# Optimization experiments

Measured on AMD Instinct MI355X. Metric: run time of the kernel, lower is better.

## Reference

```python
import jax, jax.numpy as jnp
import numpy as np

K = 1024      # num_embeddings
D = 256       # embedding_dim
BETA = 0.25
DECAY = 0.99
EPS = 1e-05


def setup_inputs() -> dict:
    key = jax.random.key(0)
    k1, k2 = jax.random.split(key)
    z_e = jax.random.normal(k1, (32, D, 32, 32), dtype=jnp.float32)
    embedding = jax.random.normal(k2, (K, D), dtype=jnp.float32)
    ema_cluster_size = jnp.zeros((K,), dtype=jnp.float32)
    ema_w = embedding  # buffer initialized as a clone of the codebook
    return {"z_e": z_e, "embedding": embedding,
            "ema_cluster_size": ema_cluster_size, "ema_w": ema_w}


def reference(z_e, embedding, ema_cluster_size, ema_w):
    B, Dd, H, W = z_e.shape
    # (B, D, H, W) -> (N, D)
    flat_z = jnp.transpose(z_e, (0, 2, 3, 1)).reshape(-1, Dd)

    # L2 distance argmin (||z||^2 + ||e||^2 - 2 z.e)
    dist = (jnp.sum(flat_z * flat_z, axis=1, keepdims=True)
            + jnp.sum(embedding * embedding, axis=1)
            - 2.0 * flat_z @ embedding.T)
    indices = jnp.argmin(dist, axis=1)  # (N,)

    # EMA update (operates on detached values; buffers updated in-place in torch)
    flat_z_sg = jax.lax.stop_gradient(flat_z)
    cluster_size = jax.ops.segment_sum(
        jnp.ones_like(indices, dtype=z_e.dtype), indices, num_segments=K)
    new_ema_cluster_size = DECAY * ema_cluster_size + (1.0 - DECAY) * cluster_size
    dw = jax.ops.segment_sum(flat_z_sg, indices, num_segments=K)  # one_hot.T @ flat_z
    new_ema_w = DECAY * ema_w + (1.0 - DECAY) * dw
    new_embedding = new_ema_w / (new_ema_cluster_size + EPS)[:, None]

    # Gather uses the *updated* codebook (torch copies into the buffer first)
    z_q_flat = new_embedding[indices]                      # (N, D)
    z_q = jnp.transpose(z_q_flat.reshape(B, H, W, Dd), (0, 3, 1, 2))

    # Straight-through estimator + commitment loss
    z_q_st = z_e + jax.lax.stop_gradient(z_q - z_e)
    vq_loss = BETA * jnp.mean((z_e - jax.lax.stop_gradient(z_q)) ** 2)

    return (z_q_st, vq_loss, indices.reshape(B, H, W),
            new_embedding, new_ema_cluster_size, new_ema_w)
```

## Files before the change

kernel.cpp:

```cpp
#include <hip/hip_runtime.h>
#include <stdint.h>

#define N_ROWS 32768
#define K_CODES 1024
#define D_DIM 256
#define NELEM 8388608

#define WS_COUNTS 0
#define WS_LOSS 1030
#define WS_ENORM 263168
#define WS_ROWBEST_BYTES 1056768
#define WS_IDX_BYTES 1318912

#define O_ZQ 0
#define O_LOSS 8388608
#define O_IDX 8388609
#define O_EMB 8421377
#define O_CS 8683521
#define O_EMAW 8684545

#define EP_BYTE_OFF 33685520

typedef _Float16 half8 __attribute__((ext_vector_type(8)));
typedef float f32x16 __attribute__((ext_vector_type(16)));

__device__ __forceinline__ unsigned int fenc(float f) {
    unsigned int u = __float_as_uint(f);
    return (u & 0x80000000u) ? ~u : (u | 0x80000000u);
}
__device__ __forceinline__ unsigned long long umin64(unsigned long long a, unsigned long long b) {
    return a < b ? a : b;
}
__device__ __forceinline__ void gll16(const void* g, void* l) {
    __builtin_amdgcn_global_load_lds((const __attribute__((address_space(1))) void*)g,
                                     (__attribute__((address_space(3))) void*)l, 16, 0, 0);
}

__global__ __launch_bounds__(256) void k_init(float* ws) {
    int i = blockIdx.x * 256 + threadIdx.x;
    if (i < 2048) ws[i] = 0.0f;
    unsigned long long* rb = (unsigned long long*)((char*)ws + WS_ROWBEST_BYTES);
    if (i < N_ROWS) rb[i] = 0xFFFFFFFFFFFFFFFFull;
}

__global__ __launch_bounds__(256) void k_conv_e(const float* __restrict__ emb,
                                                _Float16* __restrict__ Ep,
                                                float* __restrict__ enorm) {
    int k = blockIdx.x, d = threadIdx.x;
    float v = emb[k * 256 + d];
    _Float16 h = (_Float16)v;
    _Float16 l = (_Float16)(v - (float)h);
    int s = d >> 3, sub = d & 7;
    Ep[((size_t)s * 1024 + k) * 8 + sub] = h;
    Ep[((size_t)(32 + s) * 1024 + k) * 8 + sub] = l;
    float sq = v * v;
    #pragma unroll
    for (int off = 32; off >= 1; off >>= 1) sq += __shfl_down(sq, off, 64);
    __shared__ float red[4];
    if ((d & 63) == 0) red[d >> 6] = sq;
    __syncthreads();
    if (d == 0) enorm[k] = (red[0] + red[1]) + (red[2] + red[3]);
}

__global__ __launch_bounds__(256) void k_conv_z(const float* __restrict__ z_e,
                                                _Float16* __restrict__ Zp,
                                                float* __restrict__ lossacc) {
    __shared__ float lt[64 * 68];
    __shared__ float red[4];
    int t = threadIdx.x;
    int hw0 = blockIdx.x * 64, d0 = blockIdx.y * 64, b = blockIdx.z;
    const float* src = z_e + (size_t)b * 262144 + (size_t)d0 * 1024 + hw0;
    int dl = t >> 4, hl = (t & 15) * 4;
    float sq = 0.0f;
    #pragma unroll
    for (int i = 0; i < 4; i++) {
        int d = dl + i * 16;
        float4 v = *(const float4*)(src + (size_t)d * 1024 + hl);
        sq += v.x * v.x + v.y * v.y + v.z * v.z + v.w * v.w;
        lt[(hl + 0) * 68 + d] = v.x;
        lt[(hl + 1) * 68 + d] = v.y;
        lt[(hl + 2) * 68 + d] = v.z;
        lt[(hl + 3) * 68 + d] = v.w;
    }
    __syncthreads();
    int hr = t >> 2, seg = t & 3;
    int n = b * 1024 + hw0 + hr;
    int sg0 = (d0 >> 3) + seg * 2;
    half8 hi[2], lo[2];
    #pragma unroll
    for (int p = 0; p < 2; p++) {
        #pragma unroll
        for (int j = 0; j < 8; j++) {
            float v = lt[hr * 68 + seg * 16 + p * 8 + j];
            _Float16 h = (_Float16)v;
            hi[p][j] = h;
            lo[p][j] = (_Float16)(v - (float)h);
        }
    }
    *(half8*)(Zp + ((size_t)(sg0 + 0) * 32768 + n) * 8) = hi[0];
    *(half8*)(Zp + ((size_t)(sg0 + 1) * 32768 + n) * 8) = hi[1];
    *(half8*)(Zp + ((size_t)(32 + sg0) * 32768 + n) * 8) = lo[0];
    *(half8*)(Zp + ((size_t)(33 + sg0) * 32768 + n) * 8) = lo[1];
    #pragma unroll
    for (int off = 32; off >= 1; off >>= 1) sq += __shfl_down(sq, off, 64);
    if ((t & 63) == 0) red[t >> 6] = sq;
    __syncthreads();
    if (t == 0) atomicAdd(lossacc, (red[0] + red[1]) + (red[2] + red[3]));
}

__global__ __launch_bounds__(256) void k_mm(const _Float16* __restrict__ Zp,
                                            const _Float16* __restrict__ Ep,
                                            const float* __restrict__ enorm,
                                            unsigned long long* __restrict__ row_best) {
    __shared__ __align__(16) char smem[32768];
    _Float16* Za = (_Float16*)smem;
    _Float16* Ea = (_Float16*)(smem + 16384);
    unsigned long long* slot = (unsigned long long*)smem;

    int t = threadIdx.x;
    int lane = t & 63, wv = t >> 6;
    int b = blockIdx.x;
    int rt = (b & 7) + ((b >> 6) << 3);
    int ct = (b >> 3) & 7;
    int row0 = rt * 128, code0 = ct * 128;

    int wr = wv >> 1, wc = wv & 1;
    int m31 = lane & 31, ko = lane >> 5;

    f32x16 acc[2][2];
    #pragma unroll
    for (int i = 0; i < 2; i++)
        #pragma unroll
        for (int j = 0; j < 2; j++)
            #pragma unroll
            for (int r = 0; r < 16; r++) acc[i][j][r] = 0.0f;

    const char* zgl = (const char*)Zp + ((size_t)(2 * wv) * 32768 + row0 + lane) * 16;
    const char* egl = (const char*)Ep + ((size_t)(2 * wv) * 1024 + code0 + lane) * 16;
    _Float16* zld = Za + 2 * wv * 1024;
    _Float16* eld = Ea + 2 * wv * 1024;

    for (int c = 0; c < 12; c++) {
        int kz = (c < 8) ? c : (c - 8);
        int ge = (c < 4) ? c * 8 : (c < 8) ? (c - 4) * 8 : 32 + (c - 8) * 8;
        const char* zg = zgl + (size_t)kz * 8 * 32768 * 16;
        const char* eg = egl + (size_t)ge * 1024 * 16;
        gll16(zg, zld);
        gll16(zg + 64 * 16, zld + 512);
        gll16(zg + 32768 * 16, zld + 1024);
        gll16(zg + 32768 * 16 + 64 * 16, zld + 1536);
        gll16(eg, eld);
        gll16(eg + 64 * 16, eld + 512);
        gll16(eg + 1024 * 16, eld + 1024);
        gll16(eg + 1024 * 16 + 64 * 16, eld + 1536);
        __syncthreads();
        #pragma unroll
        for (int ks = 0; ks < 4; ks++) {
            int sseg = 2 * ks + ko;
            half8 a0 = *(const half8*)(Za + sseg * 1024 + (wr * 64 + m31) * 8);
            half8 a1 = *(const half8*)(Za + sseg * 1024 + (wr * 64 + 32 + m31) * 8);
            half8 b0 = *(const half8*)(Ea + sseg * 1024 + (wc * 64 + m31) * 8);
            half8 b1 = *(const half8*)(Ea + sseg * 1024 + (wc * 64 + 32 + m31) * 8);
            acc[0][0] = __builtin_amdgcn_mfma_f32_32x32x16_f16(a0, b0, acc[0][0], 0, 0, 0);
            acc[0][1] = __builtin_amdgcn_mfma_f32_32x32x16_f16(a0, b1, acc[0][1], 0, 0, 0);
            acc[1][0] = __builtin_amdgcn_mfma_f32_32x32x16_f16(a1, b0, acc[1][0], 0, 0, 0);
            acc[1][1] = __builtin_amdgcn_mfma_f32_32x32x16_f16(a1, b1, acc[1][1], 0, 0, 0);
        }
        __syncthreads();
    }

    float en0 = enorm[code0 + wc * 64 + m31];
    float en1 = enorm[code0 + wc * 64 + 32 + m31];
    unsigned int col0 = code0 + wc * 64 + m31;
    unsigned int col1 = col0 + 32;

    if (wc == 0) {
        #pragma unroll
        for (int mt = 0; mt < 2; mt++)
            #pragma unroll
            for (int j = 0; j < 16; j++) {
                int row = wr * 64 + mt * 32 + 4 * ko + (j & 3) + 8 * (j >> 2);
                unsigned long long p0 = ((unsigned long long)fenc(en0 - 2.0f * acc[mt][0][j]) << 32) | col0;
                unsigned long long p1 = ((unsigned long long)fenc(en1 - 2.0f * acc[mt][1][j]) << 32) | col1;
                slot[row * 32 + ((m31 + row) & 31)] = umin64(p0, p1);
            }
    }
    __syncthreads();
    if (wc == 1) {
        #pragma unroll
        for (int mt = 0; mt < 2; mt++)
            #pragma unroll
            for (int j = 0; j < 16; j++) {
                int row = wr * 64 + mt * 32 + 4 * ko + (j & 3) + 8 * (j >> 2);
                unsigned long long p0 = ((unsigned long long)fenc(en0 - 2.0f * acc[mt][0][j]) << 32) | col0;
                unsigned long long p1 = ((unsigned long long)fenc(en1 - 2.0f * acc[mt][1][j]) << 32) | col1;
                atomicMin(&slot[row * 32 + ((m31 + row) & 31)], umin64(p0, p1));
            }
    }
    __syncthreads();
    if (t < 128) {
        unsigned long long m = slot[t * 32 + (t & 31)];
        #pragma unroll
        for (int i = 1; i < 32; i++) m = umin64(m, slot[t * 32 + ((i + t) & 31)]);
        atomicMin(&row_best[row0 + t], m);
    }
}

__global__ __launch_bounds__(256) void k_fin_idx(const unsigned long long* __restrict__ rb,
                                                 int* __restrict__ idxs,
                                                 float* __restrict__ counts,
                                                 float* __restrict__ out) {
    __shared__ float hist[K_CODES];
    int t = threadIdx.x;
    #pragma unroll
    for (int j = 0; j < 4; j++) hist[j * 256 + t] = 0.0f;
    __syncthreads();
    int i = blockIdx.x * 256 + t;
    int id = (int)(rb[i] & 0xFFFFFFFFull);
    idxs[i] = id;
    out[O_IDX + i] = (float)id;
    atomicAdd(&hist[id], 1.0f);
    __syncthreads();
    #pragma unroll
    for (int j = 0; j < 4; j++) {
        float h = hist[j * 256 + t];
        if (h != 0.0f) atomicAdd(&counts[j * 256 + t], h);
    }
}

__global__ __launch_bounds__(256) void k_dw(const float* __restrict__ z_e,
                                            const int* __restrict__ idxs,
                                            float* __restrict__ part) {
    __shared__ float acc[K_CODES];
    int t = threadIdx.x;
    int s = blockIdx.x;
    int d = blockIdx.y;
    #pragma unroll
    for (int j = 0; j < 4; j++) acc[j * 256 + t] = 0.0f;
    __syncthreads();
    #pragma unroll
    for (int i = 0; i < 4; i++) {
        int b = s * 4 + i;
        int4 id4 = *(const int4*)(idxs + b * 1024 + t * 4);
        float4 v = *(const float4*)(z_e + (size_t)b * 262144 + (size_t)d * 1024 + t * 4);
        atomicAdd(&acc[id4.x], v.x);
        atomicAdd(&acc[id4.y], v.y);
        atomicAdd(&acc[id4.z], v.z);
        atomicAdd(&acc[id4.w], v.w);
    }
    __syncthreads();
    float* pr = part + ((size_t)s * 256 + d) * 1024;
    #pragma unroll
    for (int j = 0; j < 4; j++) pr[j * 256 + t] = acc[j * 256 + t];
}

__global__ __launch_bounds__(256) void k_red(const float* __restrict__ part,
                                             const float* __restrict__ ema_cs,
                                             const float* __restrict__ ema_w,
                                             const float* __restrict__ counts,
                                             float* __restrict__ lossacc,
                                             float* __restrict__ out) {
    __shared__ float tile[64 * 69];
    __shared__ float csl[64];
    __shared__ float craw[64];
    __shared__ float red[4];
    int t = threadIdx.x;
    int k0 = blockIdx.x * 64, d0 = blockIdx.y * 64;
    int dr = t >> 4, kc = t & 15;
    float4 sum[4] = {};
    for (int s = 0; s < 8; s++) {
        const float* pb = part + ((size_t)s * 256 + d0) * 1024 + k0 + kc * 4;
        #pragma unroll
        for (int q = 0; q < 4; q++) {
            float4 v = *(const float4*)(pb + (size_t)(dr + 16 * q) * 1024);
            sum[q].x += v.x; sum[q].y += v.y; sum[q].z += v.z; sum[q].w += v.w;
        }
    }
    if (t < 64) {
        float c = counts[k0 + t];
        craw[t] = c;
        csl[t] = 0.99f * ema_cs[k0 + t] + 0.01f * c;
    }
    #pragma unroll
    for (int q = 0; q < 4; q++) {
        float* p = tile + (dr + 16 * q) * 69 + kc * 4;
        p[0] = sum[q].x; p[1] = sum[q].y; p[2] = sum[q].z; p[3] = sum[q].w;
    }
    __syncthreads();
    int kk = t >> 2, dq = t & 3;
    int k = k0 + kk;
    float inv = 1.0f / (csl[kk] + 1e-5f);
    float cr = craw[kk];
    float lterm = 0.0f;
    #pragma unroll
    for (int j4 = 0; j4 < 4; j4++) {
        int dd = dq * 16 + j4 * 4;
        size_t kd = (size_t)k * 256 + d0 + dd;
        float4 w = *(const float4*)(ema_w + kd);
        float s0 = tile[(dd + 0) * 69 + kk];
        float s1 = tile[(dd + 1) * 69 + kk];
        float s2 = tile[(dd + 2) * 69 + kk];
        float s3 = tile[(dd + 3) * 69 + kk];
        float4 nw;
        nw.x = 0.99f * w.x + 0.01f * s0;
        nw.y = 0.99f * w.y + 0.01f * s1;
        nw.z = 0.99f * w.z + 0.01f * s2;
        nw.w = 0.99f * w.w + 0.01f * s3;
        *(float4*)(out + O_EMAW + kd) = nw;
        float4 ne = {nw.x * inv, nw.y * inv, nw.z * inv, nw.w * inv};
        *(float4*)(out + O_EMB + kd) = ne;
        lterm += ne.x * (cr * ne.x - 2.0f * s0);
        lterm += ne.y * (cr * ne.y - 2.0f * s1);
        lterm += ne.z * (cr * ne.z - 2.0f * s2);
        lterm += ne.w * (cr * ne.w - 2.0f * s3);
    }
    if (blockIdx.y == 0 && t < 64) out[O_CS + k0 + t] = csl[t];
    #pragma unroll
    for (int off = 32; off >= 1; off >>= 1) lterm += __shfl_down(lterm, off, 64);
    if ((t & 63) == 0) red[t >> 6] = lterm;
    __syncthreads();
    if (t == 0) atomicAdd(lossacc, (red[0] + red[1]) + (red[2] + red[3]));
}

__global__ __launch_bounds__(256) void k_bcast(const int* __restrict__ idxs,
                                               const float* __restrict__ lossacc,
                                               float* __restrict__ out) {
    __shared__ float lt[64 * 68];
    __shared__ int sid[64];
    int t = threadIdx.x;
    int hw0 = blockIdx.x * 64, d0 = blockIdx.y * 64, b = blockIdx.z;
    if (t < 64) sid[t] = idxs[b * 1024 + hw0 + t];
    __syncthreads();
    int r = t >> 2, c = t & 3;
    const float* nrow = out + O_EMB + (size_t)sid[r] * 256 + d0;
    #pragma unroll
    for (int it = 0; it < 4; it++) {
        int dd = it * 16 + c * 4;
        float4 q = *(const float4*)(nrow + dd);
        float* p = lt + r * 68 + dd;
        p[0] = q.x; p[1] = q.y; p[2] = q.z; p[3] = q.w;
    }
    __syncthreads();
    int dl = t >> 4, hl = (t & 15) * 4;
    float* dst = out + O_ZQ + (size_t)b * 262144 + (size_t)d0 * 1024 + hw0;
    #pragma unroll
    for (int i = 0; i < 4; i++) {
        int d = dl + i * 16;
        float4 w;
        w.x = lt[(hl + 0) * 68 + d];
        w.y = lt[(hl + 1) * 68 + d];
        w.z = lt[(hl + 2) * 68 + d];
        w.w = lt[(hl + 3) * 68 + d];
        *(float4*)(dst + (size_t)d * 1024 + hl) = w;
    }
    if (blockIdx.x == 0 && blockIdx.y == 0 && blockIdx.z == 0 && t == 0)
        out[O_LOSS] = lossacc[0] * 2.9802322387695312e-08f;
}

extern "C" void kernel_launch(void* const* d_in, const int* in_sizes, int n_in,
                              void* d_out, int out_size, void* d_ws, size_t ws_size,
                              hipStream_t stream) {
    const float* z_e = (const float*)d_in[0];
    const float* emb = (const float*)d_in[1];
    const float* ema_cs = (const float*)d_in[2];
    const float* ema_w = (const float*)d_in[3];
    float* out = (float*)d_out;
    float* ws = (float*)d_ws;

    float* counts = ws + WS_COUNTS;
    float* lossacc = ws + WS_LOSS;
    float* enorm = ws + WS_ENORM;
    unsigned long long* row_best = (unsigned long long*)((char*)d_ws + WS_ROWBEST_BYTES);
    int* idxs = (int*)((char*)d_ws + WS_IDX_BYTES);

    _Float16* Zp = (_Float16*)d_out;
    _Float16* Ep = (_Float16*)((char*)d_out + EP_BYTE_OFF);
    float* part = (float*)d_out;

    k_init<<<128, 256, 0, stream>>>(ws);
    k_conv_e<<<1024, 256, 0, stream>>>(emb, Ep, enorm);
    k_conv_z<<<dim3(16, 4, 32), 256, 0, stream>>>(z_e, Zp, lossacc);
    k_mm<<<2048, 256, 0, stream>>>(Zp, Ep, enorm, row_best);
    k_fin_idx<<<128, 256, 0, stream>>>(row_best, idxs, counts, out);
    k_dw<<<dim3(8, 256), 256, 0, stream>>>(z_e, idxs, part);
    k_red<<<dim3(16, 4), 256, 0, stream>>>(part, ema_cs, ema_w, counts, lossacc, out);
    k_bcast<<<dim3(16, 4, 32), 256, 0, stream>>>(idxs, lossacc, out);
}
```

Measured before the change: 245.6 us.

## Enlarge distance GEMM tiles to 256x256 with double-buffered LDS prefetch

Reworks the distance-matmul kernel to use 512-thread blocks computing 256x256 tiles, so each wave holds a 4x2 grid of MFMA accumulators. Global-to-LDS loads are double-buffered, with the next K chunk issued while the current one is computed, and fine-grained vmcnt waits and raw barriers replace full __syncthreads. The block index is remapped for locality. The aim is more operand reuse and hidden load latency, at the cost of 128KB of LDS (one block per CU) and more accumulator registers.

```diff
diff --git a/kernel.cpp b/kernel.cpp
--- a/kernel.cpp
+++ b/kernel.cpp
@@ -108,67 +108,91 @@
     if (t == 0) atomicAdd(lossacc, (red[0] + red[1]) + (red[2] + red[3]));
 }
 
-__global__ __launch_bounds__(256) void k_mm(const _Float16* __restrict__ Zp,
+__global__ __launch_bounds__(512) void k_mm(const _Float16* __restrict__ Zp,
                                             const _Float16* __restrict__ Ep,
                                             const float* __restrict__ enorm,
                                             unsigned long long* __restrict__ row_best) {
-    __shared__ __align__(16) char smem[32768];
-    _Float16* Za = (_Float16*)smem;
-    _Float16* Ea = (_Float16*)(smem + 16384);
-    unsigned long long* slot = (unsigned long long*)smem;
+    __shared__ __align__(16) char smem[131072];
 
     int t = threadIdx.x;
     int lane = t & 63, wv = t >> 6;
     int b = blockIdx.x;
-    int rt = (b & 7) + ((b >> 6) << 3);
-    int ct = (b >> 3) & 7;
-    int row0 = rt * 128, code0 = ct * 128;
-
-    int wr = wv >> 1, wc = wv & 1;
+    int wgid = (b & 7) * 64 + (b >> 3);
+    int rt = wgid >> 2;
+    int ct = wgid & 3;
+    int row0 = rt * 256, code0 = ct * 256;
+
+    int wr = wv >> 2, wc = wv & 3;
     int m31 = lane & 31, ko = lane >> 5;
 
-    f32x16 acc[2][2];
-    #pragma unroll
-    for (int i = 0; i < 2; i++)
-        #pragma unroll
-        for (int j = 0; j < 2; j++)
+    f32x16 acc[4][2];
+    #pragma unroll
+    for (int m = 0; m < 4; m++)
+        #pragma unroll
+        for (int n = 0; n < 2; n++)
             #pragma unroll
-            for (int r = 0; r < 16; r++) acc[i][j][r] = 0.0f;
-
-    const char* zgl = (const char*)Zp + ((size_t)(2 * wv) * 32768 + row0 + lane) * 16;
-    const char* egl = (const char*)Ep + ((size_t)(2 * wv) * 1024 + code0 + lane) * 16;
-    _Float16* zld = Za + 2 * wv * 1024;
-    _Float16* eld = Ea + 2 * wv * 1024;
-
-    for (int c = 0; c < 12; c++) {
+            for (int r = 0; r < 16; r++) acc[m][n][r] = 0.0f;
+
+    const char* zbase = (const char*)Zp + ((size_t)wv * 32768 + row0 + lane) * 16;
+    const char* ebase = (const char*)Ep + ((size_t)wv * 1024 + code0 + lane) * 16;
+    _Float16* zlds = (_Float16*)smem + wv * 256 * 8;
+    _Float16* elds = (_Float16*)(smem + 32768) + wv * 256 * 8;
+
+    auto STAGE = [&](int c, int buf) {
         int kz = (c < 8) ? c : (c - 8);
         int ge = (c < 4) ? c * 8 : (c < 8) ? (c - 4) * 8 : 32 + (c - 8) * 8;
-        const char* zg = zgl + (size_t)kz * 8 * 32768 * 16;
-        const char* eg = egl + (size_t)ge * 1024 * 16;
-        gll16(zg, zld);
-        gll16(zg + 64 * 16, zld + 512);
-        gll16(zg + 32768 * 16, zld + 1024);
-        gll16(zg + 32768 * 16 + 64 * 16, zld + 1536);
-        gll16(eg, eld);
-        gll16(eg + 64 * 16, eld + 512);
-        gll16(eg + 1024 * 16, eld + 1024);
-        gll16(eg + 1024 * 16 + 64 * 16, eld + 1536);
-        __syncthreads();
+        const char* zg = zbase + (size_t)kz * 8 * 32768 * 16;
+        const char* eg = ebase + (size_t)ge * 1024 * 16;
+        _Float16* zl = zlds + buf * 32768;
+        _Float16* el = elds + buf * 32768;
+        #pragma unroll
+        for (int i = 0; i < 4; i++) {
+            gll16(zg + (size_t)i * 64 * 16, zl + i * 512);
+            gll16(eg + (size_t)i * 64 * 16, el + i * 512);
+        }
+    };
+
+    STAGE(0, 0);
+    STAGE(1, 1);
+    asm volatile("s_waitcnt vmcnt(8)" ::: "memory");
+    __builtin_amdgcn_s_barrier();
+    asm volatile("" ::: "memory");
+
+    for (int c = 0; c < 12; c++) {
+        const _Float16* Za = (const _Float16*)(smem + (c & 1) * 65536);
+        const _Float16* Ea = (const _Float16*)(smem + (c & 1) * 65536 + 32768);
+        __builtin_amdgcn_s_setprio(1);
         #pragma unroll
         for (int ks = 0; ks < 4; ks++) {
             int sseg = 2 * ks + ko;
-            half8 a0 = *(const half8*)(Za + sseg * 1024 + (wr * 64 + m31) * 8);
-            half8 a1 = *(const half8*)(Za + sseg * 1024 + (wr * 64 + 32 + m31) * 8);
-            half8 b0 = *(const half8*)(Ea + sseg * 1024 + (wc * 64 + m31) * 8);
-            half8 b1 = *(const half8*)(Ea + sseg * 1024 + (wc * 64 + 32 + m31) * 8);
+            half8 a0 = *(const half8*)(Za + (sseg * 256 + wr * 128 +  0 + m31) * 8);
+            half8 a1 = *(const half8*)(Za + (sseg * 256 + wr * 128 + 32 + m31) * 8);
+            half8 a2 = *(const half8*)(Za + (sseg * 256 + wr * 128 + 64 + m31) * 8);
+            half8 a3 = *(const half8*)(Za + (sseg * 256 + wr * 128 + 96 + m31) * 8);
+            half8 b0 = *(const half8*)(Ea + (sseg * 256 + wc * 64 +  0 + m31) * 8);
+            half8 b1 = *(const half8*)(Ea + (sseg * 256 + wc * 64 + 32 + m31) * 8);
             acc[0][0] = __builtin_amdgcn_mfma_f32_32x32x16_f16(a0, b0, acc[0][0], 0, 0, 0);
             acc[0][1] = __builtin_amdgcn_mfma_f32_32x32x16_f16(a0, b1, acc[0][1], 0, 0, 0);
             acc[1][0] = __builtin_amdgcn_mfma_f32_32x32x16_f16(a1, b0, acc[1][0], 0, 0, 0);
             acc[1][1] = __builtin_amdgcn_mfma_f32_32x32x16_f16(a1, b1, acc[1][1], 0, 0, 0);
+            acc[2][0] = __builtin_amdgcn_mfma_f32_32x32x16_f16(a2, b0, acc[2][0], 0, 0, 0);
+            acc[2][1] = __builtin_amdgcn_mfma_f32_32x32x16_f16(a2, b1, acc[2][1], 0, 0, 0);
+            acc[3][0] = __builtin_amdgcn_mfma_f32_32x32x16_f16(a3, b0, acc[3][0], 0, 0, 0);
+            acc[3][1] = __builtin_amdgcn_mfma_f32_32x32x16_f16(a3, b1, acc[3][1], 0, 0, 0);
         }
-        __syncthreads();
-    }
-
+        __builtin_amdgcn_s_setprio(0);
+        asm volatile("s_waitcnt lgkmcnt(0)" ::: "memory");
+        __builtin_amdgcn_s_barrier();
+        if (c < 10) STAGE(c + 2, c & 1);
+        if (c < 11) {
+            if (c < 10) asm volatile("s_waitcnt vmcnt(8)" ::: "memory");
+            else        asm volatile("s_waitcnt vmcnt(0)" ::: "memory");
+            __builtin_amdgcn_s_barrier();
+            asm volatile("" ::: "memory");
+        }
+    }
+
+    unsigned long long* slot = (unsigned long long*)smem;
     float en0 = enorm[code0 + wc * 64 + m31];
     float en1 = enorm[code0 + wc * 64 + 32 + m31];
     unsigned int col0 = code0 + wc * 64 + m31;
@@ -176,33 +200,33 @@
 
     if (wc == 0) {
         #pragma unroll
-        for (int mt = 0; mt < 2; mt++)
+        for (int m = 0; m < 4; m++)
             #pragma unroll
             for (int j = 0; j < 16; j++) {
-                int row = wr * 64 + mt * 32 + 4 * ko + (j & 3) + 8 * (j >> 2);
-                unsigned long long p0 = ((unsigned long long)fenc(en0 - 2.0f * acc[mt][0][j]) << 32) | col0;
-                unsigned long long p1 = ((unsigned long long)fenc(en1 - 2.0f * acc[mt][1][j]) << 32) | col1;
+                int row = wr * 128 + m * 32 + 4 * ko + (j & 3) + 8 * (j >> 2);
+                unsigned long long p0 = ((unsigned long long)fenc(en0 - 2.0f * acc[m][0][j]) << 32) | col0;
+                unsigned long long p1 = ((unsigned long long)fenc(en1 - 2.0f * acc[m][1][j]) << 32) | col1;
                 slot[row * 32 + ((m31 + row) & 31)] = umin64(p0, p1);
             }
     }
     __syncthreads();
-    if (wc == 1) {
-        #pragma unroll
-        for (int mt = 0; mt < 2; mt++)
+    if (wc != 0) {
+        #pragma unroll
+        for (int m = 0; m < 4; m++)
             #pragma unroll
             for (int j = 0; j < 16; j++) {
-                int row = wr * 64 + mt * 32 + 4 * ko + (j & 3) + 8 * (j >> 2);
-                unsigned long long p0 = ((unsigned long long)fenc(en0 - 2.0f * acc[mt][0][j]) << 32) | col0;
-                unsigned long long p1 = ((unsigned long long)fenc(en1 - 2.0f * acc[mt][1][j]) << 32) | col1;
+                int row = wr * 128 + m * 32 + 4 * ko + (j & 3) + 8 * (j >> 2);
+                unsigned long long p0 = ((unsigned long long)fenc(en0 - 2.0f * acc[m][0][j]) << 32) | col0;
+                unsigned long long p1 = ((unsigned long long)fenc(en1 - 2.0f * acc[m][1][j]) << 32) | col1;
                 atomicMin(&slot[row * 32 + ((m31 + row) & 31)], umin64(p0, p1));
             }
     }
     __syncthreads();
-    if (t < 128) {
-        unsigned long long m = slot[t * 32 + (t & 31)];
-        #pragma unroll
-        for (int i = 1; i < 32; i++) m = umin64(m, slot[t * 32 + ((i + t) & 31)]);
-        atomicMin(&row_best[row0 + t], m);
+    if (t < 256) {
+        unsigned long long mm = slot[t * 32 + (t & 31)];
+        #pragma unroll
+        for (int i = 1; i < 32; i++) mm = umin64(mm, slot[t * 32 + ((i + t) & 31)]);
+        atomicMin(&row_best[row0 + t], mm);
     }
 }
 
@@ -380,7 +404,7 @@
     k_init<<<128, 256, 0, stream>>>(ws);
     k_conv_e<<<1024, 256, 0, stream>>>(emb, Ep, enorm);
     k_conv_z<<<dim3(16, 4, 32), 256, 0, stream>>>(z_e, Zp, lossacc);
-    k_mm<<<2048, 256, 0, stream>>>(Zp, Ep, enorm, row_best);
+    k_mm<<<512, 512, 0, stream>>>(Zp, Ep, enorm, row_best);
     k_fin_idx<<<128, 256, 0, stream>>>(row_best, idxs, counts, out);
     k_dw<<<dim3(8, 256), 256, 0, stream>>>(z_e, idxs, part);
     k_red<<<dim3(16, 4), 256, 0, stream>>>(part, ema_cs, ema_w, counts, lossacc, out);
```

Result: no change. 244.2 us (-0.6%).
